# Kernel tuning notes

Measured on AMD Instinct MI355X. Metric: run time of the kernel, lower is better.

Reference implementation:

```python
import jax, jax.numpy as jnp
import numpy as np

N = 50000   # nodes
E = 400000  # edges (before self-loops)
F = 128     # num_features
H = 8       # heads (layer 1)
C = 64      # hidden_channels
B = 64      # graphs in batch
K = 10      # num_classes
NEG_SLOPE = 0.2


def setup_inputs() -> dict:
    key = jax.random.key(0)
    ks = jax.random.split(key, 12)
    g = lambda k, shape, fan: jax.random.normal(k, shape, jnp.float32) / np.sqrt(fan).astype(np.float32)
    return {
        "x": jax.random.normal(ks[0], (N, F), jnp.float32),
        "edge_index": jax.random.randint(ks[1], (2, E), 0, N, jnp.int32),
        "batch": jnp.sort(jax.random.randint(ks[2], (N,), 0, B, jnp.int32)),
        "W1": g(ks[3], (F, H * C), F),
        "att_src1": g(ks[4], (H, C), C),
        "att_dst1": g(ks[5], (H, C), C),
        "b1": jnp.zeros((H * C,), jnp.float32),
        "W2": g(ks[6], (H * C, C), H * C),
        "att_src2": g(ks[7], (1, C), C),
        "att_dst2": g(ks[8], (1, C), C),
        "b2": jnp.zeros((C,), jnp.float32),
        "lin1_w": g(ks[9], (C, C), C),
        "lin1_b": jnp.zeros((C,), jnp.float32),
        "lin2_w": g(ks[10], (C, K), C),
        "lin2_b": jnp.zeros((K,), jnp.float32),
    }


def gat_conv(x, src, dst, W, att_src, att_dst, bias):
    """PyG GATConv (self-loops already appended to src/dst). x:[N,Fin] -> [N,H*C]."""
    heads, out_c = att_src.shape
    h = (x @ W).reshape(N, heads, out_c)                      # [N,H,C]
    a_s = jnp.einsum('nhc,hc->nh', h, att_src)                # [N,H]
    a_d = jnp.einsum('nhc,hc->nh', h, att_dst)
    e = jax.nn.leaky_relu(a_s[src] + a_d[dst], NEG_SLOPE)     # [E',H]
    # segment softmax over incoming edges of each destination node
    m = jax.ops.segment_max(e, dst, num_segments=N)
    e = jnp.exp(e - m[dst])
    denom = jax.ops.segment_sum(e, dst, num_segments=N)
    alpha = e / (denom[dst] + 1e-16)                          # [E',H]
    out = jax.ops.segment_sum(h[src] * alpha[:, :, None], dst, num_segments=N)  # [N,H,C]
    return out.reshape(N, heads * out_c) + bias


def reference(x, edge_index, batch, W1, att_src1, att_dst1, b1,
              W2, att_src2, att_dst2, b2, lin1_w, lin1_b, lin2_w, lin2_b):
    loops = jnp.arange(N, dtype=edge_index.dtype)
    src = jnp.concatenate([edge_index[0], loops])
    dst = jnp.concatenate([edge_index[1], loops])

    h = gat_conv(x, src, dst, W1, att_src1, att_dst1, b1)     # [N, H*C]
    h = jax.nn.elu(h)                                         # dropout inactive (eval)
    h = gat_conv(h, src, dst, W2, att_src2, att_dst2, b2)     # [N, C]
    h = jax.nn.elu(h)

    pooled = jax.ops.segment_sum(h, batch, num_segments=B)    # global_add_pool -> [B, C]
    z = jax.nn.elu(pooled @ lin1_w + lin1_b)
    logits = z @ lin2_w + lin2_b
    return jax.nn.log_softmax(logits, axis=-1)
```

## Files before the change

### kernel.cpp

```cpp
#include <hip/hip_runtime.h>
#include <hip/hip_bf16.h>

#define DEV static __device__ __forceinline__

constexpr int F1 = 128;
constexpr int H1 = 8;
constexpr int C  = 64;
constexpr int B  = 64;
constexpr int K  = 10;
constexpr float NEG = 0.2f;
constexpr unsigned SMASK = 0x07FFFFFFu;

typedef __attribute__((ext_vector_type(8))) short short8;
typedef __attribute__((ext_vector_type(4))) float floatx4;

DEV float b2f(__hip_bfloat16 x) { return __bfloat162float(x); }
DEV float elu1(float v) { return v > 0.f ? v : (__expf(v) - 1.f); }
DEV unsigned short f2bbits(float f) {
  __hip_bfloat16 b = __float2bfloat16(f);
  return *(unsigned short*)&b;
}
DEV float blo(unsigned u) { return __uint_as_float(u << 16); }
DEV float bhi(unsigned u) { return __uint_as_float(u & 0xffff0000u); }
DEV float bu(unsigned short u) { return __uint_as_float(((unsigned)u) << 16); }
DEV unsigned pack2(float lo, float hi) {
  return (unsigned)f2bbits(lo) | ((unsigned)f2bbits(hi) << 16);
}
DEV float rcp_nr(float x) {
  float r = __builtin_amdgcn_rcpf(x);
  return r * (2.f - x * r);
}


DEV int detect_dev(const void* xraw, int* lds) {
  if (threadIdx.x == 0) {
    const __hip_bfloat16* xb = (const __hip_bfloat16*)xraw;
    int bad = 0;
    for (int i = 0; i < 128; ++i) {
      float v = b2f(xb[2 * i]);
      if (!(fabsf(v) < 1e4f)) bad++;
    }
    *lds = (bad < 13) ? 1 : 0;
  }
  __syncthreads();
  return *lds;
}

#define CVT(p, i) (isbf ? b2f(((const __hip_bfloat16*)(p))[i]) : ((const float*)(p))[i])

__global__ void fused_prep_kernel(const void* x_raw, const void* w1raw,
                                  const void* as1r, const void* ad1r, const void* b1r,
                                  const void* w2raw,
                                  const void* as2r, const void* ad2r, const void* b2r,
                                  const void* l1wr, const void* l1br,
                                  const void* l2wr, const void* l2br,
                                  unsigned short* __restrict__ xbf,
                                  unsigned short* __restrict__ w1frag,
                                  unsigned short* __restrict__ w2frag,
                                  unsigned short* __restrict__ vfrag,
                                  float* __restrict__ wts,
                                  int* __restrict__ deg,
                                  float* __restrict__ pooled,
                                  int nX, int N) {
  __shared__ int fl;
  int isbf = detect_dev(x_raw, &fl);
  int gid = blockIdx.x * 256 + threadIdx.x;
  int stride = gridDim.x * 256;

  int ng = nX >> 3;
  if (isbf) {
    const uint4* src = (const uint4*)x_raw;
    uint4* dst = (uint4*)xbf;
    for (int i = gid; i < ng; i += stride) dst[i] = src[i];
  } else {
    const float4* src = (const float4*)x_raw;
    uint4* dst = (uint4*)xbf;
    for (int i = gid; i < ng; i += stride) {
      float4 a = src[2 * i], b = src[2 * i + 1];
      uint4 o;
      o.x = pack2(a.x, a.y); o.y = pack2(a.z, a.w);
      o.z = pack2(b.x, b.y); o.w = pack2(b.z, b.w);
      dst[i] = o;
    }
  }
  for (int i = ng * 8 + gid; i < nX; i += stride)
    xbf[i] = isbf ? ((const unsigned short*)x_raw)[i]
                  : f2bbits(((const float*)x_raw)[i]);

  for (int i = gid; i < 512;  i += stride) {
    int hp = i >> 7, l16 = (i >> 3) & 15, nt = i & 7;
    int c = hp * 128 + nt * 16 + l16;
    wts[1024 + i] = CVT(b1r, c);
  }
  for (int i = gid; i < 64;   i += stride) wts[1536 + i] = CVT(as2r, i);
  for (int i = gid; i < 64;   i += stride) wts[1600 + i] = CVT(ad2r, i);
  for (int i = gid; i < 64;   i += stride) wts[1664 + i] = CVT(b2r, i);
  for (int i = gid; i < 4096; i += stride) wts[1728 + i] = CVT(l1wr, i);
  for (int i = gid; i < 64;   i += stride) wts[5824 + i] = CVT(l1br, i);
  for (int i = gid; i < 640;  i += stride) wts[5888 + i] = CVT(l2wr, i);
  for (int i = gid; i < 10;   i += stride) wts[6528 + i] = CVT(l2br, i);
  for (int t = gid; t < 8192; t += stride) {
    int lane = t & 63, ks = (t >> 6) & 3, nt = t >> 8;
    for (int j = 0; j < 8; ++j) {
      int k = ks * 32 + (lane >> 4) * 8 + j;
      int n = nt * 16 + (lane & 15);
      w1frag[t * 8 + j] = f2bbits(CVT(w1raw, k * 512 + n));
    }
  }
  for (int t = gid; t < 4096; t += stride) {
    int lane = t & 63, nt = (t >> 6) & 3, ks = t >> 8;
    for (int j = 0; j < 8; ++j) {
      int p = ks * 32 + (lane >> 4) * 8 + j;
      int hp = p >> 7, pl16 = (p >> 3) & 15, pnt = p & 7;
      int k = hp * 128 + pnt * 16 + pl16;
      int n = nt * 16 + (lane & 15);
      w2frag[t * 8 + j] = f2bbits(CVT(w2raw, k * 64 + n));
    }
  }
  for (int t = gid; t < 2048; t += stride) {
    int j = t & 7, lane = (t >> 3) & 63, ks = t >> 9;
    int k = ks * 32 + (lane >> 4) * 8 + j;
    int n = lane & 15;
    int hh = (n < 8) ? n : (n - 8);
    float s = 0.f;
    if (n < 8) {
      for (int c = 0; c < 64; ++c)
        s += CVT(w1raw, k * 512 + hh * 64 + c) * CVT(as1r, hh * 64 + c);
    } else {
      for (int c = 0; c < 64; ++c)
        s += CVT(w1raw, k * 512 + hh * 64 + c) * CVT(ad1r, hh * 64 + c);
    }
    vfrag[(ks * 64 + lane) * 8 + j] = f2bbits(s);
  }
  for (int i = gid; i < N; i += stride) deg[i] = 0;
  for (int i = gid; i < B * C; i += stride) pooled[i] = 0.f;
}

__global__ __launch_bounds__(256) void deg_att_kernel(
    const int* __restrict__ ei, int E, int Etot, int* __restrict__ deg,
    const unsigned short* __restrict__ xbf,
    const unsigned short* __restrict__ vfrag,
    float* __restrict__ a_s, float* __restrict__ a_d,
    int N, int attBlocks) {
  if ((int)blockIdx.x >= attBlocks) {
    int e = ((int)blockIdx.x - attBlocks) * 256 + threadIdx.x;
    if (e < Etot) {
      int d = (e < E) ? ei[E + e] : e - E;
      atomicAdd(&deg[d], 1);
    }
    return;
  }
  int t = threadIdx.x, w = t >> 6, lane = t & 63;
  int quad = lane >> 4, l16 = lane & 15;
  int row0 = blockIdx.x * 64 + w * 16;

  floatx4 acc = {};
  int rl = row0 + l16; if (rl >= N) rl = N - 1;
  const unsigned short* xp = xbf + (size_t)rl * 128 + quad * 8;
#pragma unroll
  for (int ks = 0; ks < 4; ++ks) {
    short8 a = *(const short8*)(xp + ks * 32);
    short8 b = *(const short8*)&vfrag[(ks * 64 + lane) * 8];
    acc = __builtin_amdgcn_mfma_f32_16x16x32_bf16(a, b, acc, 0, 0, 0);
  }
#pragma unroll
  for (int r = 0; r < 4; ++r) {
    int row = row0 + quad * 4 + r;
    if (row < N) {
      if (l16 < 8) a_s[(size_t)row * 8 + l16] = acc[r];
      else         a_d[(size_t)row * 8 + (l16 - 8)] = acc[r];
    }
  }
}

__global__ void scan_block_kernel(const int* __restrict__ deg,
                                  int* __restrict__ local,
                                  int* __restrict__ bsum, int N) {
  __shared__ int tmp[256];
  int t = threadIdx.x;
  int i = blockIdx.x * 256 + t;
  int v = (i < N) ? deg[i] : 0;
  tmp[t] = v;
  __syncthreads();
  for (int off = 1; off < 256; off <<= 1) {
    int u = (t >= off) ? tmp[t - off] : 0;
    __syncthreads();
    tmp[t] += u;
    __syncthreads();
  }
  if (i < N) local[i] = tmp[t] - v;
  if (t == 255) bsum[blockIdx.x] = tmp[255];
}

__global__ void scan_finish_kernel(const int* __restrict__ local,
                                   const int* __restrict__ bsum, int nb,
                                   int* __restrict__ rowptr,
                                   int* __restrict__ cursor, int N, int Etot) {
  __shared__ int tmp[256];
  __shared__ int offs;
  int t = threadIdx.x;
  int v0 = (t < nb) ? bsum[t] : 0;
  tmp[t] = v0;
  __syncthreads();
  for (int off = 1; off < 256; off <<= 1) {
    int u = (t >= off) ? tmp[t - off] : 0;
    __syncthreads();
    tmp[t] += u;
    __syncthreads();
  }
  if (t == (int)blockIdx.x) offs = tmp[t] - v0;
  __syncthreads();
  int i = blockIdx.x * 256 + t;
  if (i < N) {
    int r = local[i] + offs;
    rowptr[i] = r;
    cursor[i] = r;
  }
  if (i == 0) rowptr[N] = Etot;
}

__global__ void fill_weight_kernel(const int* __restrict__ ei, int E, int Etot,
                                   const float* __restrict__ a_s,
                                   const float* __restrict__ a_d,
                                   int* __restrict__ cursor,
                                   int* __restrict__ col,
                                   unsigned short* __restrict__ wedge) {
  int e = blockIdx.x * 256 + threadIdx.x;
  if (e >= Etot) return;
  int s, d;
  if (e < E) { s = ei[e]; d = ei[E + e]; } else { s = d = e - E; }
  int pos = atomicAdd(&cursor[d], 1);
  col[pos] = s | ((d & 15) << 27);
  float4 s0 = *(const float4*)(a_s + (size_t)s * 8);
  float4 s1 = *(const float4*)(a_s + (size_t)s * 8 + 4);
  float4 d0 = *(const float4*)(a_d + (size_t)d * 8);
  float4 d1 = *(const float4*)(a_d + (size_t)d * 8 + 4);
  float v, w0, w1, w2, w3, w4, w5, w6, w7;
  v = s0.x + d0.x; v = v > 0.f ? v : NEG * v; w0 = __expf(v);
  v = s0.y + d0.y; v = v > 0.f ? v : NEG * v; w1 = __expf(v);
  v = s0.z + d0.z; v = v > 0.f ? v : NEG * v; w2 = __expf(v);
  v = s0.w + d0.w; v = v > 0.f ? v : NEG * v; w3 = __expf(v);
  v = s1.x + d1.x; v = v > 0.f ? v : NEG * v; w4 = __expf(v);
  v = s1.y + d1.y; v = v > 0.f ? v : NEG * v; w5 = __expf(v);
  v = s1.z + d1.z; v = v > 0.f ? v : NEG * v; w6 = __expf(v);
  v = s1.w + d1.w; v = v > 0.f ? v : NEG * v; w7 = __expf(v);
  uint4 o;
  o.x = pack2(w0, w1); o.y = pack2(w2, w3);
  o.z = pack2(w4, w5); o.w = pack2(w6, w7);
  *(uint4*)(wedge + (size_t)pos * 8) = o;
}

__global__ __launch_bounds__(512, 6) void aggx_gemm1_kernel(
    const unsigned short* __restrict__ xbf,
    const unsigned short* __restrict__ W1frag,
    const int* __restrict__ rowptr,
    const int* __restrict__ col,
    const unsigned short* __restrict__ wedge,
    const float* __restrict__ bias_perm,
    unsigned short* __restrict__ out1,
    int N) {
  __shared__ __align__(16) char LB[8 * 16 * 136 * 2];
  unsigned short* AggP = (unsigned short*)LB;

  int t = threadIdx.x, w = t >> 6, lane = t & 63;
  int q = lane >> 4, n = lane & 15;
  int dbase = blockIdx.x * 16;

  int R0 = rowptr[dbase];
  int R1 = rowptr[min(dbase + 16, N)];
  int nch = (R1 - R0 + 31) >> 5;

  int kp = t >> 5, pp = t & 31;
  int skey = (pp & 7) << 4;
  int dw = t >> 5, kw = t & 31;

  short8 onesf = {};
  if (n == 0) {
#pragma unroll
    for (int j = 0; j < 8; ++j) onesf[j] = (short)0x3F80;
  }

  floatx4 accw[8] = {};
  floatx4 accdn = {};

  uint2 pxa, pxb;
  uint4 pwv;
  int pcv;
  {
    int e0 = R0 + 2 * kp;
    int ec0 = min(e0, R1 - 1), ec1 = min(e0 + 1, R1 - 1);
    int s0 = col[ec0] & SMASK;
    int s1 = col[ec1] & SMASK;
    pxa = *(const uint2*)(xbf + (size_t)s0 * 128 + pp * 4);
    pxb = *(const uint2*)(xbf + (size_t)s1 * 128 + pp * 4);
    int ew = min(R0 + kw, R1 - 1);
    pcv = col[ew];
    pwv = *(const uint4*)(wedge + (size_t)ew * 8);
  }

  for (int c = 0; c < nch; ++c) {
    char* Lb = LB + (c & 1) * 16384;
    unsigned short* XgTc = (unsigned short*)Lb;
    unsigned short* Wmc  = (unsigned short*)(Lb + 8192);

    {
      int base = 256 * pp + 4 * kp;
      unsigned w0 = (pxa.x & 0xffffu) | (pxb.x << 16);
      unsigned w1 = (pxa.x >> 16) | (pxb.x & 0xffff0000u);
      unsigned w2 = (pxa.y & 0xffffu) | (pxb.y << 16);
      unsigned w3 = (pxa.y >> 16) | (pxb.y & 0xffff0000u);
      *(unsigned*)(Lb + ((base)       ^ skey)) = w0;
      *(unsigned*)(Lb + ((base + 64)  ^ skey)) = w1;
      *(unsigned*)(Lb + ((base + 128) ^ skey)) = w2;
      *(unsigned*)(Lb + ((base + 192) ^ skey)) = w3;

      int ew = R0 + c * 32 + kw;
      int dl = (pcv >> 27) & 15;
      bool mine = (ew < R1) && (dl == dw);
      unsigned short* wmp = Wmc + dw * 32 + kw;
      wmp[0]    = mine ? (unsigned short)(pwv.x & 0xffff) : 0;
      wmp[512]  = mine ? (unsigned short)(pwv.x >> 16)    : 0;
      wmp[1024] = mine ? (unsigned short)(pwv.y & 0xffff) : 0;
      wmp[1536] = mine ? (unsigned short)(pwv.y >> 16)    : 0;
      wmp[2048] = mine ? (unsigned short)(pwv.z & 0xffff) : 0;
      wmp[2560] = mine ? (unsigned short)(pwv.z >> 16)    : 0;
      wmp[3072] = mine ? (unsigned short)(pwv.w & 0xffff) : 0;
      wmp[3584] = mine ? (unsigned short)(pwv.w >> 16)    : 0;
    }
    if (c + 1 < nch) {
      int ebase = R0 + (c + 1) * 32;
      int e0 = ebase + 2 * kp;
      int ec0 = min(e0, R1 - 1), ec1 = min(e0 + 1, R1 - 1);
      int s0 = col[ec0] & SMASK;
      int s1 = col[ec1] & SMASK;
      pxa = *(const uint2*)(xbf + (size_t)s0 * 128 + pp * 4);
      pxb = *(const uint2*)(xbf + (size_t)s1 * 128 + pp * 4);
      int ew = min(ebase + kw, R1 - 1);
      pcv = col[ew];
      pwv = *(const uint4*)(wedge + (size_t)ew * 8);
    }
    __syncthreads();

    short8 af = *(const short8*)(Wmc + w * 512 + n * 32 + 8 * q);
    accdn = __builtin_amdgcn_mfma_f32_16x16x32_bf16(af, onesf, accdn, 0, 0, 0);
#pragma unroll
    for (int ft = 0; ft < 8; ++ft) {
      int f = ft * 16 + n;
      int bb = f * 64 + 16 * q;
      bb ^= ((f >> 2) & 7) << 4;
      short8 bfr = *(const short8*)((const char*)XgTc + bb);
      accw[ft] = __builtin_amdgcn_mfma_f32_16x16x32_bf16(af, bfr, accw[ft], 0, 0, 0);
    }
  }

  __syncthreads();

  {
    float dnv[4];
#pragma unroll
    for (int r = 0; r < 4; ++r) {
      float dr = __shfl(accdn[r], lane & 48);
      dnv[r] = rcp_nr(dr + 1e-16f);
    }
#pragma unroll
    for (int ft = 0; ft < 8; ++ft)
#pragma unroll
      for (int r = 0; r < 4; ++r)
        AggP[w * 2176 + (4 * q + r) * 136 + ft * 16 + n] =
            f2bbits(accw[ft][r] * dnv[r]);
  }
  __syncthreads();

  {
    int hp = w >> 1, qq = w & 1;
    floatx4 acc2[4] = {};
    const unsigned short* Bp = W1frag + (size_t)hp * 16384;
#pragma unroll
    for (int ks = 0; ks < 4; ++ks) {
      short8 a2 = *(const short8*)&AggP[w * 2176 + n * 136 + ks * 32 + q * 8];
#pragma unroll
      for (int j = 0; j < 4; ++j) {
        int nt = qq * 4 + j;
        short8 b2 = *(const short8*)&Bp[((nt * 4 + ks) * 64 + lane) * 8];
        acc2[j] = __builtin_amdgcn_mfma_f32_16x16x32_bf16(a2, b2, acc2[j], 0, 0, 0);
      }
    }
    float4 bq = *(const float4*)&bias_perm[hp * 128 + n * 8 + qq * 4];
#pragma unroll
    for (int r = 0; r < 4; ++r) {
      int row = dbase + 4 * q + r;
      if (row < N) {
        uint2 o;
        o.x = pack2(elu1(acc2[0][r] + bq.x), elu1(acc2[1][r] + bq.y));
        o.y = pack2(elu1(acc2[2][r] + bq.z), elu1(acc2[3][r] + bq.w));
        *(uint2*)&out1[(size_t)row * 512 + hp * 128 + n * 8 + qq * 4] = o;
      }
    }
  }
}

__global__ __launch_bounds__(256) void gemm2_mfma_kernel(
    const unsigned short* __restrict__ x2bf,
    const unsigned short* __restrict__ W2frag,
    const float* __restrict__ att_src,
    const float* __restrict__ att_dst,
    unsigned short* __restrict__ h2,
    float* __restrict__ a_s, float* __restrict__ a_d,
    int N) {
  int t = threadIdx.x;
  int w = t >> 6, lane = t & 63;
  int quad = lane >> 4, l16 = lane & 15;
  int rowbase = blockIdx.x * 64 + w * 16;

  floatx4 acc[4] = {};
  int r0 = rowbase + l16; if (r0 >= N) r0 = N - 1;
  const unsigned short* p0 = x2bf + (size_t)r0 * 512 + quad * 8;
#pragma unroll
  for (int ks = 0; ks < 16; ++ks) {
    short8 a0 = *(const short8*)(p0 + ks * 32);
#pragma unroll
    for (int nt = 0; nt < 4; ++nt) {
      short8 b = *(const short8*)&W2frag[((ks * 4 + nt) * 64 + lane) * 8];
      acc[nt] = __builtin_amdgcn_mfma_f32_16x16x32_bf16(a0, b, acc[nt], 0, 0, 0);
    }
  }

  float asw[4], adw[4];
#pragma unroll
  for (int nt = 0; nt < 4; ++nt) {
    asw[nt] = att_src[nt * 16 + l16];
    adw[nt] = att_dst[nt * 16 + l16];
  }
  float ps[4] = {}, pd[4] = {};
#pragma unroll
  for (int nt = 0; nt < 4; ++nt)
#pragma unroll
    for (int r = 0; r < 4; ++r) {
      float v = acc[nt][r];
      int row = rowbase + quad * 4 + r;
      if (row < N) h2[(size_t)row * 64 + nt * 16 + l16] = f2bbits(v);
      ps[r] += v * asw[nt];
      pd[r] += v * adw[nt];
    }
#pragma unroll
  for (int r = 0; r < 4; ++r) {
    float p = ps[r], q = pd[r];
#pragma unroll
    for (int off = 1; off < 16; off <<= 1) {
      p += __shfl_xor(p, off);
      q += __shfl_xor(q, off);
    }
    int row = rowbase + quad * 4 + r;
    if (l16 == 0 && row < N) {
      a_s[row] = p;
      a_d[row] = q;
    }
  }
}

__global__ void gat_agg1_kernel(const int* __restrict__ rowptr,
                                const int* __restrict__ col,
                                const float* __restrict__ a_s,
                                const float* __restrict__ a_d,
                                const unsigned short* __restrict__ hfeat,
                                const float* __restrict__ bias,
                                unsigned short* __restrict__ out, int N) {
  int wave = threadIdx.x >> 6, lane = threadIdx.x & 63;
  int d = blockIdx.x * 4 + wave;
  if (d >= N) return;
  int beg = rowptr[d], end = rowptr[d + 1];
  int qg = lane >> 4, l16 = lane & 15;
  float adv = a_d[d];
  const uint2* hfu = (const uint2*)hfeat;
  float acc[4] = {};
  float wsum = 0.f;
#pragma unroll 2
  for (int i = beg + qg; i < end; i += 4) {
    int s = col[i] & SMASK;
    float v = a_s[s] + adv;
    v = v > 0.f ? v : NEG * v;
    float wv = __expf(v);
    wsum += wv;
    uint2 u = hfu[(size_t)s * 16 + l16];
    acc[0] += wv * blo(u.x); acc[1] += wv * bhi(u.x);
    acc[2] += wv * blo(u.y); acc[3] += wv * bhi(u.y);
  }
#pragma unroll
  for (int off = 16; off <= 32; off <<= 1) {
#pragma unroll
    for (int j = 0; j < 4; ++j) acc[j] += __shfl_xor(acc[j], off);
    wsum += __shfl_xor(wsum, off);
  }
  float winv = 1.f / (wsum + 1e-16f);
  float4 bb = ((const float4*)bias)[l16];
  float r0 = elu1(acc[0] * winv + bb.x), r1 = elu1(acc[1] * winv + bb.y);
  float r2 = elu1(acc[2] * winv + bb.z), r3 = elu1(acc[3] * winv + bb.w);
  if (qg == 0) {
    uint2 o; o.x = pack2(r0, r1); o.y = pack2(r2, r3);
    ((uint2*)out)[(size_t)d * 16 + l16] = o;
  }
}

__global__ void pool_kernel(const unsigned short* __restrict__ out2,
                            const int* __restrict__ batch,
                            float* __restrict__ pooled, int N) {
  int wave = threadIdx.x >> 6, lane = threadIdx.x & 63;
  int seg = blockIdx.x * 4 + wave;
  int start = seg * 16;
  if (start >= N) return;
  int end = min(start + 16, N);
  int cur = batch[start];
  float acc = 0.f;
  for (int n = start; n < end; ++n) {
    int bn = batch[n];
    if (bn != cur) {
      unsafeAtomicAdd(&pooled[cur * 64 + lane], acc);
      acc = 0.f; cur = bn;
    }
    acc += bu(out2[(size_t)n * 64 + lane]);
  }
  unsafeAtomicAdd(&pooled[cur * 64 + lane], acc);
}

__global__ void head_kernel(const float* __restrict__ pooled,
                            const float* __restrict__ lin1_w,
                            const float* __restrict__ lin1_b,
                            const float* __restrict__ lin2_w,
                            const float* __restrict__ lin2_b,
                            const void* __restrict__ x_raw,
                            void* __restrict__ outv) {
  __shared__ float P[C];
  __shared__ float Zs[C];
  __shared__ float Ls[K];
  __shared__ float lse_s;
  __shared__ int fl;
  int isbf = detect_dev(x_raw, &fl);
  int g = blockIdx.x, t = threadIdx.x;
  P[t] = pooled[g * C + t];
  __syncthreads();
  float acc = lin1_b[t];
  for (int k = 0; k < C; ++k) acc += P[k] * lin1_w[k * C + t];
  Zs[t] = elu1(acc);
  __syncthreads();
  if (t < K) {
    float a = lin2_b[t];
    for (int k = 0; k < C; ++k) a += Zs[k] * lin2_w[k * K + t];
    Ls[t] = a;
  }
  __syncthreads();
  if (t == 0) {
    float mx = -1e30f;
    for (int c = 0; c < K; ++c) mx = fmaxf(mx, Ls[c]);
    float s = 0.f;
    for (int c = 0; c < K; ++c) s += __expf(Ls[c] - mx);
    lse_s = mx + __logf(s);
  }
  __syncthreads();
  if (t < K) {
    float val = Ls[t] - lse_s;
    if (isbf) ((__hip_bfloat16*)outv)[g * K + t] = __float2bfloat16(val);
    else      ((float*)outv)[g * K + t] = val;
  }
}

extern "C" void kernel_launch(void* const* d_in, const int* in_sizes, int n_in,
                              void* d_out, int out_size, void* d_ws, size_t ws_size,
                              hipStream_t stream) {
  const void* x_raw = d_in[0];
  const int*  ei    = (const int*)d_in[1];
  const int*  batch = (const int*)d_in[2];

  const int N    = in_sizes[2];
  const int E    = in_sizes[1] / 2;
  const int Etot = E + N;
  const int nb   = (N + 255) / 256;

  float* ws   = (float*)d_ws;
  size_t off  = 0;

  float* wts = ws + off; off += 6544;
  float* b1w  = wts + 1024;
  float* as2w = wts + 1536;
  float* ad2w = wts + 1600;
  float* b2w  = wts + 1664;
  float* l1w  = wts + 1728;
  float* l1b  = wts + 5824;
  float* l2w  = wts + 5888;
  float* l2b  = wts + 6528;

  unsigned short* xbf    = (unsigned short*)(ws + off); off += (size_t)N * 64;
  unsigned short* w1frag = (unsigned short*)(ws + off); off += 32768;
  unsigned short* w2frag = (unsigned short*)(ws + off); off += 16384;
  unsigned short* vfrag  = (unsigned short*)(ws + off); off += 1024;
  unsigned short* wedge  = (unsigned short*)(ws + off); off += (size_t)Etot * 4;
  unsigned short* out1bf = (unsigned short*)(ws + off); off += (size_t)N * 256;
  unsigned short* h2bf   = (unsigned short*)(ws + off); off += (size_t)N * 32;
  unsigned short* out2bf = (unsigned short*)(ws + off); off += (size_t)N * 32;
  float* as1  = ws + off; off += (size_t)N * H1;
  float* ad1  = ws + off; off += (size_t)N * H1;
  float* as2  = ws + off; off += (size_t)N;
  float* ad2  = ws + off; off += (size_t)N;
  float* pooled = ws + off; off += (size_t)B * C;

  int* ibase  = (int*)(ws + off);
  int* deg    = ibase;                 ibase += N;
  int* cursor = ibase;                 ibase += N;
  int* rowptr = ibase;                 ibase += N + 1;
  int* locals = ibase;                 ibase += N;
  int* bsum   = ibase;                 ibase += 256;
  int* col    = ibase;                 ibase += Etot;

  fused_prep_kernel<<<1024, 256, 0, stream>>>(
      x_raw, d_in[3], d_in[4], d_in[5], d_in[6], d_in[7], d_in[8], d_in[9],
      d_in[10], d_in[11], d_in[12], d_in[13], d_in[14],
      xbf, w1frag, w2frag, vfrag, wts, deg, pooled, in_sizes[0], N);

  {
    int attBlocks = (N + 63) / 64;
    int degBlocks = (Etot + 255) / 256;
    deg_att_kernel<<<attBlocks + degBlocks, 256, 0, stream>>>(
        ei, E, Etot, deg, xbf, vfrag, as1, ad1, N, attBlocks);
  }

  scan_block_kernel<<<nb, 256, 0, stream>>>(deg, locals, bsum, N);
  scan_finish_kernel<<<nb, 256, 0, stream>>>(locals, bsum, nb, rowptr, cursor, N, Etot);

  fill_weight_kernel<<<(Etot + 255) / 256, 256, 0, stream>>>(
      ei, E, Etot, as1, ad1, cursor, col, wedge);

  aggx_gemm1_kernel<<<(N + 15) / 16, 512, 0, stream>>>(
      xbf, w1frag, rowptr, col, wedge, b1w, out1bf, N);

  gemm2_mfma_kernel<<<(N + 63) / 64, 256, 0, stream>>>(out1bf, w2frag, as2w, ad2w,
                                                       h2bf, as2, ad2, N);
  gat_agg1_kernel<<<(N + 3) / 4, 256, 0, stream>>>(rowptr, col, as2, ad2, h2bf, b2w, out2bf, N);

  pool_kernel<<<(N + 63) / 64, 256, 0, stream>>>(out2bf, batch, pooled, N);
  head_kernel<<<B, 64, 0, stream>>>(pooled, l1w, l1b, l2w, l2b, x_raw, (void*)d_out);
}
```

Before: 284.4 us.

## Fuse layer-2 GEMM and attention logits into layer-1 aggregation kernel

Merges the second GAT layer's linear transform and attention-score computation into the layer-1 aggregate+GEMM kernel. The ELU'd layer-1 output for each 16-node tile now stays in shared memory, and a split-K MFMA across 8 waves with a shared-memory reduction produces h2, a_s2 and a_d2. This removes the N×512 bf16 intermediate write and read plus one kernel launch. In exchange it adds extra syncthreads, LDS atomics and more work per block, and only 16-row tiles feed the second GEMM.

```diff
diff --git a/kernel.cpp b/kernel.cpp
--- a/kernel.cpp
+++ b/kernel.cpp
@@ -250,17 +250,20 @@
   *(uint4*)(wedge + (size_t)pos * 8) = o;
 }
 
-__global__ __launch_bounds__(512, 6) void aggx_gemm1_kernel(
+__global__ __launch_bounds__(512, 6) void aggx_gemm12_kernel(
     const unsigned short* __restrict__ xbf,
     const unsigned short* __restrict__ W1frag,
     const int* __restrict__ rowptr,
     const int* __restrict__ col,
     const unsigned short* __restrict__ wedge,
     const float* __restrict__ bias_perm,
-    unsigned short* __restrict__ out1,
+    const unsigned short* __restrict__ W2frag,
+    const float* __restrict__ att_src2,
+    const float* __restrict__ att_dst2,
+    unsigned short* __restrict__ h2,
+    float* __restrict__ a_s2, float* __restrict__ a_d2,
     int N) {
   __shared__ __align__(16) char LB[8 * 16 * 136 * 2];
-  unsigned short* AggP = (unsigned short*)LB;
 
   int t = threadIdx.x, w = t >> 6, lane = t & 63;
   int q = lane >> 4, n = lane & 15;
@@ -355,6 +358,7 @@
 
   __syncthreads();
 
+  unsigned short* AggP = (unsigned short*)LB;
   {
     float dnv[4];
 #pragma unroll
@@ -371,9 +375,9 @@
   }
   __syncthreads();
 
+  int hp = w >> 1, qq = w & 1;
+  floatx4 acc2[4] = {};
   {
-    int hp = w >> 1, qq = w & 1;
-    floatx4 acc2[4] = {};
     const unsigned short* Bp = W1frag + (size_t)hp * 16384;
 #pragma unroll
     for (int ks = 0; ks < 4; ++ks) {
@@ -385,75 +389,75 @@
         acc2[j] = __builtin_amdgcn_mfma_f32_16x16x32_bf16(a2, b2, acc2[j], 0, 0, 0);
       }
     }
-    float4 bq = *(const float4*)&bias_perm[hp * 128 + n * 8 + qq * 4];
+  }
+  float4 bq = *(const float4*)&bias_perm[hp * 128 + n * 8 + qq * 4];
+  __syncthreads();
+
+  unsigned short* O1 = (unsigned short*)LB;
+  float* RED = (float*)(LB + 16640);
+  float* PSb = (float*)(LB + 20736);
+  float* PDb = (float*)(LB + 20800);
+
+  {
 #pragma unroll
     for (int r = 0; r < 4; ++r) {
+      int dl = 4 * q + r;
+      unsigned short* op = O1 + dl * 520 + hp * 128 + n * 8 + qq * 4;
+      op[0] = f2bbits(elu1(acc2[0][r] + bq.x));
+      op[1] = f2bbits(elu1(acc2[1][r] + bq.y));
+      op[2] = f2bbits(elu1(acc2[2][r] + bq.z));
+      op[3] = f2bbits(elu1(acc2[3][r] + bq.w));
+    }
+    if (t < 32) ((float*)(LB + 20736))[t] = 0.f;
+  }
+  __syncthreads();
+
+  int nt2 = w & 3, kh = w >> 2;
+  floatx4 acc3 = {};
+#pragma unroll
+  for (int ks8 = 0; ks8 < 8; ++ks8) {
+    int ks = kh * 8 + ks8;
+    short8 a3 = *(const short8*)&O1[n * 520 + ks * 32 + q * 8];
+    short8 b3 = *(const short8*)&W2frag[((ks * 4 + nt2) * 64 + lane) * 8];
+    acc3 = __builtin_amdgcn_mfma_f32_16x16x32_bf16(a3, b3, acc3, 0, 0, 0);
+  }
+  if (kh == 1) *(floatx4*)&RED[(nt2 * 64 + lane) * 4] = acc3;
+  __syncthreads();
+
+  if (kh == 0) {
+    floatx4 other = *(const floatx4*)&RED[(nt2 * 64 + lane) * 4];
+    float asw = att_src2[nt2 * 16 + n];
+    float adw = att_dst2[nt2 * 16 + n];
+    float ps[4], pd[4];
+#pragma unroll
+    for (int r = 0; r < 4; ++r) {
+      float v = acc3[r] + other[r];
       int row = dbase + 4 * q + r;
-      if (row < N) {
-        uint2 o;
-        o.x = pack2(elu1(acc2[0][r] + bq.x), elu1(acc2[1][r] + bq.y));
-        o.y = pack2(elu1(acc2[2][r] + bq.z), elu1(acc2[3][r] + bq.w));
-        *(uint2*)&out1[(size_t)row * 512 + hp * 128 + n * 8 + qq * 4] = o;
+      if (row < N) h2[(size_t)row * 64 + nt2 * 16 + n] = f2bbits(v);
+      ps[r] = v * asw;
+      pd[r] = v * adw;
+    }
+#pragma unroll
+    for (int r = 0; r < 4; ++r) {
+      float p = ps[r], qd = pd[r];
+#pragma unroll
+      for (int off2 = 1; off2 < 16; off2 <<= 1) {
+        p += __shfl_xor(p, off2);
+        qd += __shfl_xor(qd, off2);
       }
-    }
-  }
-}
-
-__global__ __launch_bounds__(256) void gemm2_mfma_kernel(
-    const unsigned short* __restrict__ x2bf,
-    const unsigned short* __restrict__ W2frag,
-    const float* __restrict__ att_src,
-    const float* __restrict__ att_dst,
-    unsigned short* __restrict__ h2,
-    float* __restrict__ a_s, float* __restrict__ a_d,
-    int N) {
-  int t = threadIdx.x;
-  int w = t >> 6, lane = t & 63;
-  int quad = lane >> 4, l16 = lane & 15;
-  int rowbase = blockIdx.x * 64 + w * 16;
-
-  floatx4 acc[4] = {};
-  int r0 = rowbase + l16; if (r0 >= N) r0 = N - 1;
-  const unsigned short* p0 = x2bf + (size_t)r0 * 512 + quad * 8;
-#pragma unroll
-  for (int ks = 0; ks < 16; ++ks) {
-    short8 a0 = *(const short8*)(p0 + ks * 32);
-#pragma unroll
-    for (int nt = 0; nt < 4; ++nt) {
-      short8 b = *(const short8*)&W2frag[((ks * 4 + nt) * 64 + lane) * 8];
-      acc[nt] = __builtin_amdgcn_mfma_f32_16x16x32_bf16(a0, b, acc[nt], 0, 0, 0);
-    }
-  }
-
-  float asw[4], adw[4];
-#pragma unroll
-  for (int nt = 0; nt < 4; ++nt) {
-    asw[nt] = att_src[nt * 16 + l16];
-    adw[nt] = att_dst[nt * 16 + l16];
-  }
-  float ps[4] = {}, pd[4] = {};
-#pragma unroll
-  for (int nt = 0; nt < 4; ++nt)
-#pragma unroll
-    for (int r = 0; r < 4; ++r) {
-      float v = acc[nt][r];
-      int row = rowbase + quad * 4 + r;
-      if (row < N) h2[(size_t)row * 64 + nt * 16 + l16] = f2bbits(v);
-      ps[r] += v * asw[nt];
-      pd[r] += v * adw[nt];
-    }
-#pragma unroll
-  for (int r = 0; r < 4; ++r) {
-    float p = ps[r], q = pd[r];
-#pragma unroll
-    for (int off = 1; off < 16; off <<= 1) {
-      p += __shfl_xor(p, off);
-      q += __shfl_xor(q, off);
-    }
-    int row = rowbase + quad * 4 + r;
-    if (l16 == 0 && row < N) {
-      a_s[row] = p;
-      a_d[row] = q;
+      if (n == 0) {
+        int dl = 4 * q + r;
+        atomicAdd(&PSb[dl], p);
+        atomicAdd(&PDb[dl], qd);
+      }
+    }
+  }
+  __syncthreads();
+  if (t < 16) {
+    int row = dbase + t;
+    if (row < N) {
+      a_s2[row] = PSb[t];
+      a_d2[row] = PDb[t];
     }
   }
 }
@@ -593,7 +597,6 @@
   unsigned short* w2frag = (unsigned short*)(ws + off); off += 16384;
   unsigned short* vfrag  = (unsigned short*)(ws + off); off += 1024;
   unsigned short* wedge  = (unsigned short*)(ws + off); off += (size_t)Etot * 4;
-  unsigned short* out1bf = (unsigned short*)(ws + off); off += (size_t)N * 256;
   unsigned short* h2bf   = (unsigned short*)(ws + off); off += (size_t)N * 32;
   unsigned short* out2bf = (unsigned short*)(ws + off); off += (size_t)N * 32;
   float* as1  = ws + off; off += (size_t)N * H1;
@@ -628,11 +631,10 @@
   fill_weight_kernel<<<(Etot + 255) / 256, 256, 0, stream>>>(
       ei, E, Etot, as1, ad1, cursor, col, wedge);
 
-  aggx_gemm1_kernel<<<(N + 15) / 16, 512, 0, stream>>>(
-      xbf, w1frag, rowptr, col, wedge, b1w, out1bf, N);
-
-  gemm2_mfma_kernel<<<(N + 63) / 64, 256, 0, stream>>>(out1bf, w2frag, as2w, ad2w,
-                                                       h2bf, as2, ad2, N);
+  aggx_gemm12_kernel<<<(N + 15) / 16, 512, 0, stream>>>(
+      xbf, w1frag, rowptr, col, wedge, b1w,
+      w2frag, as2w, ad2w, h2bf, as2, ad2, N);
+
   gat_agg1_kernel<<<(N + 3) / 4, 256, 0, stream>>>(rowptr, col, as2, ad2, h2bf, b2w, out2bf, N);
 
   pool_kernel<<<(N + 63) / 64, 256, 0, stream>>>(out2bf, batch, pooled, N);
```

Result: faster. 274.7 us (-3.4%).
